# Performance work log

Measured on AMD Instinct MI355X. Metric: run time of the kernel, lower is better.

The kernel has to match this reference:

```python
import jax, jax.numpy as jnp
import numpy as np

N_NODES = 100000
N_EDGES = 1250000
D = 64
K = 5
EPS = 1e-8


def setup_inputs() -> dict:
    key = jax.random.key(0)
    k1, k2, k3, k4 = jax.random.split(key, 4)
    x = jax.random.normal(k1, (N_NODES, D), dtype=jnp.float32)
    mask = jax.random.normal(k2, (N_NODES, 1), dtype=jnp.float32)
    edge_index = jax.random.randint(k3, (2, N_EDGES), 0, N_NODES, dtype=jnp.int64)
    # orthogonal-ish init for the linear layer (QR of gaussian), gain for tanh = 5/3
    g = jax.random.normal(k4, (D, D), dtype=jnp.float32)
    q, _ = jnp.linalg.qr(g)
    W = (5.0 / 3.0) * q.astype(jnp.float32)
    b = jnp.zeros((D,), dtype=jnp.float32)
    alpha = jnp.float32(0.001)
    return {"x": x, "mask": mask, "edge_index": edge_index, "W": W, "b": b, "alpha": alpha}


def _forward(x, mask, edge_index, W, b, alpha):
    n = x.shape[0]
    # x_fn: Linear + Tanh
    h = jnp.tanh(x @ W.T + b)  # [N, D]
    src = edge_index[0]
    dst = edge_index[1]
    hs = h[src]  # [E, D] gather
    hd = h[dst]  # [E, D] gather
    # torch cosine_similarity with eps clamp on each norm
    ns = jnp.maximum(jnp.sqrt(jnp.sum(hs * hs, axis=-1)), EPS)
    nd = jnp.maximum(jnp.sqrt(jnp.sum(hd * hd, axis=-1)), EPS)
    cos = jnp.sum(hs * hd, axis=-1) / (ns * nd)
    edge_weights = jax.nn.relu(cos)  # [E]

    # gcn_norm with self loops (PyG APPNP default): D^-1/2 (A + I) D^-1/2
    loop = jnp.arange(n, dtype=src.dtype)
    row = jnp.concatenate([src, loop])
    col = jnp.concatenate([dst, loop])
    w = jnp.concatenate([edge_weights, jnp.ones((n,), dtype=edge_weights.dtype)])
    deg = jax.ops.segment_sum(w, col, num_segments=n)
    dis = jnp.where(deg > 0, jax.lax.rsqrt(jnp.maximum(deg, EPS)), 0.0)
    norm_w = dis[row] * w * dis[col]  # [E + N]

    # APPNP: K steps of f = (1-alpha) * A_hat @ f + alpha * f0
    f0 = jax.nn.relu(mask)  # [N, 1]
    f = f0
    for _ in range(K):
        msg = norm_w[:, None] * f[row]  # gather + weight
        agg = jax.ops.segment_sum(msg, col, num_segments=n)  # scatter-add
        f = (1.0 - alpha) * agg + alpha * f0
    return f, edge_weights


def reference(x, mask, edge_index, W, b, alpha):
    return _forward(x, mask, edge_index, W, b, alpha)
```

## Files before the change

### kernel.cpp

```cpp
#include <hip/hip_runtime.h>
#include <hip/hip_fp16.h>
#include <math.h>

#define N_NODES 100000
#define N_EDGES 1250000
#define D 64
#define EPS 1e-8f

#define ZERO_BLOCKS 391
#define GEMM_BLOCKS 1024
#define NODE_BLOCKS 391
#define COSR_BLOCKS 9766

__global__ __launch_bounds__(256) void k_gemm_zero(
    const float* __restrict__ x, const float* __restrict__ W,
    const float* __restrict__ b, __half* __restrict__ hn,
    unsigned long long* __restrict__ cnt64)
{
    if (blockIdx.x < ZERO_BLOCKS) {
        int i = blockIdx.x * 256 + threadIdx.x;
        if (i < N_NODES) cnt64[i] = 0ULL;
        return;
    }
    __shared__ float xrow[4][72];
    const int lane = threadIdx.x & 63;
    const int wid  = threadIdx.x >> 6;

    float Wreg[64];
    const float4* Wv = (const float4*)(W + lane * D);
    #pragma unroll
    for (int q = 0; q < 16; ++q) {
        float4 w4 = Wv[q];
        Wreg[4*q+0] = w4.x; Wreg[4*q+1] = w4.y;
        Wreg[4*q+2] = w4.z; Wreg[4*q+3] = w4.w;
    }
    const float bj = b[lane];
    float* xl = xrow[wid];

    const int wave   = (blockIdx.x - ZERO_BLOCKS) * 4 + wid;
    const int nwaves = GEMM_BLOCKS * 4;

    for (int row = wave; row < N_NODES; row += nwaves) {
        float xv = x[(size_t)row * D + lane];
        xl[lane] = xv;
        float acc = bj;
        #pragma unroll
        for (int q = 0; q < 16; ++q) {
            float4 xk4 = *(const float4*)(xl + 4*q);
            acc = fmaf(xk4.x, Wreg[4*q+0], acc);
            acc = fmaf(xk4.y, Wreg[4*q+1], acc);
            acc = fmaf(xk4.z, Wreg[4*q+2], acc);
            acc = fmaf(xk4.w, Wreg[4*q+3], acc);
        }
        float h = tanhf(acc);
        float s = h * h;
        #pragma unroll
        for (int m = 32; m >= 1; m >>= 1) s += __shfl_xor(s, m, 64);
        float nrm = fmaxf(sqrtf(s), EPS);
        hn[(size_t)row * D + lane] = __float2half_rn(h / nrm);
    }
}

__device__ __forceinline__ float dot8h(float4 a, float4 c)
{
    const __half2* ah = (const __half2*)&a;
    const __half2* ch = (const __half2*)&c;
    float p = 0.0f;
    #pragma unroll
    for (int q = 0; q < 4; ++q) {
        float2 af = __half22float2(ah[q]);
        float2 cf = __half22float2(ch[q]);
        p = fmaf(af.x, cf.x, p);
        p = fmaf(af.y, cf.y, p);
    }
    return p;
}

__global__ __launch_bounds__(256) void k_cos_rank(
    const int* __restrict__ ei, const __half* __restrict__ hn,
    unsigned long long* __restrict__ cnt64, int* __restrict__ rank,
    float* __restrict__ wout)
{
    int t = blockIdx.x * 256 + threadIdx.x;
    int g = t >> 3, sub = t & 7;
    if (g >= N_EDGES / 4) return;
    int e0 = g * 4;
    int4 ss = *(const int4*)(ei + e0);
    int4 dd = *(const int4*)(ei + N_EDGES + e0);

    float4 a0 = ((const float4*)(hn + (size_t)ss.x * D))[sub];
    float4 c0 = ((const float4*)(hn + (size_t)dd.x * D))[sub];
    float4 a1 = ((const float4*)(hn + (size_t)ss.y * D))[sub];
    float4 c1 = ((const float4*)(hn + (size_t)dd.y * D))[sub];
    float4 a2 = ((const float4*)(hn + (size_t)ss.z * D))[sub];
    float4 c2 = ((const float4*)(hn + (size_t)dd.z * D))[sub];
    float4 a3 = ((const float4*)(hn + (size_t)ss.w * D))[sub];
    float4 c3 = ((const float4*)(hn + (size_t)dd.w * D))[sub];

    float p0 = dot8h(a0, c0);
    float p1 = dot8h(a1, c1);
    float p2 = dot8h(a2, c2);
    float p3 = dot8h(a3, c3);
    p0 += __shfl_xor(p0, 1, 64);  p1 += __shfl_xor(p1, 1, 64);
    p2 += __shfl_xor(p2, 1, 64);  p3 += __shfl_xor(p3, 1, 64);
    p0 += __shfl_xor(p0, 2, 64);  p1 += __shfl_xor(p1, 2, 64);
    p2 += __shfl_xor(p2, 2, 64);  p3 += __shfl_xor(p3, 2, 64);
    p0 += __shfl_xor(p0, 4, 64);  p1 += __shfl_xor(p1, 4, 64);
    p2 += __shfl_xor(p2, 4, 64);  p3 += __shfl_xor(p3, 4, 64);

    float w0 = fmaxf(p0, 0.0f);
    float w1 = fmaxf(p1, 0.0f);
    float w2 = fmaxf(p2, 0.0f);
    float w3 = fmaxf(p3, 0.0f);

    if (sub == 0) {
        *(float4*)(wout + e0) = make_float4(w0, w1, w2, w3);
    }
    if (sub < 4) {
        float w = (sub == 0) ? w0 : (sub == 1) ? w1 : (sub == 2) ? w2 : w3;
        int   d = (sub == 0) ? dd.x : (sub == 1) ? dd.y : (sub == 2) ? dd.z : dd.w;
        if (w > 0.0f) {
            unsigned long long pack =
                (1ULL << 40) | (unsigned long long)(w * 4294967296.0f);
            unsigned long long old = atomicAdd(cnt64 + d, pack);
            rank[e0 + sub] = (int)(old >> 40);
        }
    }
}

__device__ __forceinline__ int wave_iscan(int v, int lane)
{
    int incl = v;
    #pragma unroll
    for (int m = 1; m < 64; m <<= 1) {
        int o = __shfl_up(incl, m, 64);
        if (lane >= m) incl += o;
    }
    return incl;
}

__global__ __launch_bounds__(256) void k_scan1(
    const unsigned long long* __restrict__ cnt64, int* __restrict__ rowptr,
    int* __restrict__ bsum, const float* __restrict__ mask,
    float* __restrict__ dis, float* __restrict__ y)
{
    __shared__ int wsum[4];
    int t = threadIdx.x, b = blockIdx.x;
    int i = b * 256 + t;
    int lane = t & 63, wid = t >> 6;
    unsigned long long pv = (i < N_NODES) ? cnt64[i] : 0ULL;
    int v = (int)(pv >> 40);
    if (i < N_NODES) {
        float degsum = (float)(pv & 0xFFFFFFFFFFULL) * 2.3283064365386963e-10f;
        float di = rsqrtf(fmaxf(degsum + 1.0f, EPS));
        dis[i] = di;
        y[i] = di * fmaxf(mask[i], 0.0f);
    }
    int incl = wave_iscan(v, lane);
    if (lane == 63) wsum[wid] = incl;
    __syncthreads();
    int off = 0;
    #pragma unroll
    for (int k = 0; k < 4; ++k) if (k < wid) off += wsum[k];
    if (i < N_NODES) rowptr[i] = off + incl - v;
    if (t == 255) bsum[b] = off + incl;
}

__global__ __launch_bounds__(512) void k_scan2(
    const int* __restrict__ bsum, int* __restrict__ boff, int nblk,
    int* __restrict__ rowptr)
{
    __shared__ int wsum[8];
    int t = threadIdx.x;
    int lane = t & 63, wid = t >> 6;
    int v = (t < nblk) ? bsum[t] : 0;
    int incl = wave_iscan(v, lane);
    if (lane == 63) wsum[wid] = incl;
    __syncthreads();
    int off = 0;
    #pragma unroll
    for (int k = 0; k < 8; ++k) if (k < wid) off += wsum[k];
    if (t < nblk) boff[t] = off + incl - v;
    if (t == nblk - 1) rowptr[N_NODES] = off + incl;
}

__global__ __launch_bounds__(256) void k_place(
    const int* __restrict__ ei, const int* __restrict__ rank_pos,
    const int* __restrict__ rowptr, const int* __restrict__ boff,
    const float* __restrict__ wsrc, int2* __restrict__ pairs)
{
    int e = blockIdx.x * 256 + threadIdx.x;
    if (e >= N_EDGES) return;
    float w = wsrc[e];
    if (!(w > 0.0f)) return;
    int s = ei[e];
    int d = ei[N_EDGES + e];
    int pos = rowptr[d] + boff[d >> 8] + rank_pos[e];
    pairs[pos] = make_int2(s, __float_as_int(w));
}

__global__ __launch_bounds__(256) void k_spmv(
    const int* __restrict__ rowptr, const int* __restrict__ boff,
    const int2* __restrict__ pairs,
    const float* __restrict__ y_in, const float* __restrict__ dis,
    const float* __restrict__ mask, const float* __restrict__ alpha_p,
    float* __restrict__ y_out, float* __restrict__ f_out)
{
    int t = blockIdx.x * 256 + threadIdx.x;
    int node = t >> 2, l = t & 3;
    if (node >= N_NODES) return;
    int beg = rowptr[node] + boff[node >> 8];
    int np1 = node + 1;
    int end = rowptr[np1] + (np1 < N_NODES ? boff[np1 >> 8] : 0);
    float sum = 0.0f;
    for (int j = beg + l; j < end; j += 8) {
        int2 p0 = pairs[j];
        int j2 = j + 4;
        int2 p1 = make_int2(0, 0);
        if (j2 < end) p1 = pairs[j2];
        sum += __int_as_float(p0.y) * y_in[p0.x];
        sum += __int_as_float(p1.y) * y_in[p1.x];
    }
    sum += __shfl_xor(sum, 1, 64);
    sum += __shfl_xor(sum, 2, 64);
    if (l == 0) {
        float di = dis[node];
        float alpha = alpha_p[0];
        float f0 = fmaxf(mask[node], 0.0f);
        float fn = (1.0f - alpha) * di * (sum + y_in[node]) + alpha * f0;
        if (f_out) f_out[node] = fn;
        y_out[node] = di * fn;
    }
}

extern "C" void kernel_launch(void* const* d_in, const int* in_sizes, int n_in,
                              void* d_out, int out_size, void* d_ws, size_t ws_size,
                              hipStream_t stream)
{
    const float* x     = (const float*)d_in[0];
    const float* mask  = (const float*)d_in[1];
    const int*   ei    = (const int*)  d_in[2];
    const float* W     = (const float*)d_in[3];
    const float* b     = (const float*)d_in[4];
    const float* alpha = (const float*)d_in[5];

    float* out_f = (float*)d_out;
    float* out_w = (float*)d_out + N_NODES;

    float* ws = (float*)d_ws;
    __half* hn    = (__half*)ws;
    int2*  pairs  = (int2*) (ws + 3200000);
    int*   rank   = (int*)  (ws + 5700000);
    unsigned long long* cnt64 = (unsigned long long*)(ws + 6950000);
    int*   rowptr = (int*)  (ws + 7150000);
    float* dis    =          ws + 7250016;
    float* y_a    =          ws + 7350016;
    float* y_b    =          ws + 7450016;
    int*   bsum   = (int*)  (ws + 7550016);
    int*   boff   = (int*)  (ws + 7550528);

    const int edgeBlocks = (N_EDGES + 255) / 256;
    const int segBlocks  = (int)(((long long)N_NODES * 4 + 255) / 256);

    k_gemm_zero<<<ZERO_BLOCKS + GEMM_BLOCKS, 256, 0, stream>>>(x, W, b, hn, cnt64);
    k_cos_rank<<<COSR_BLOCKS, 256, 0, stream>>>(ei, hn, cnt64, rank, out_w);
    k_scan1<<<NODE_BLOCKS, 256, 0, stream>>>(cnt64, rowptr, bsum, mask, dis, y_a);
    k_scan2<<<1, 512, 0, stream>>>(bsum, boff, NODE_BLOCKS, rowptr);
    k_place<<<edgeBlocks, 256, 0, stream>>>(ei, rank, rowptr, boff, out_w, pairs);

    k_spmv<<<segBlocks, 256, 0, stream>>>(rowptr, boff, pairs, y_a, dis, mask, alpha, y_b, (float*)nullptr);
    k_spmv<<<segBlocks, 256, 0, stream>>>(rowptr, boff, pairs, y_b, dis, mask, alpha, y_a, (float*)nullptr);
    k_spmv<<<segBlocks, 256, 0, stream>>>(rowptr, boff, pairs, y_a, dis, mask, alpha, y_b, (float*)nullptr);
    k_spmv<<<segBlocks, 256, 0, stream>>>(rowptr, boff, pairs, y_b, dis, mask, alpha, y_a, (float*)nullptr);
    k_spmv<<<segBlocks, 256, 0, stream>>>(rowptr, boff, pairs, y_a, dis, mask, alpha, y_b, out_f);
}
```

Before: 202.8 us.

## Pack CSR pairs into 32-bit words with 15-bit quantized weights

```diff
diff --git a/kernel.cpp b/kernel.cpp
--- a/kernel.cpp
+++ b/kernel.cpp
@@ -78,7 +78,7 @@
 
 __global__ __launch_bounds__(256) void k_cos_rank(
     const int* __restrict__ ei, const __half* __restrict__ hn,
-    unsigned long long* __restrict__ cnt64, int* __restrict__ rank,
+    unsigned long long* __restrict__ cnt64, unsigned char* __restrict__ rank,
     float* __restrict__ wout)
 {
     int t = blockIdx.x * 256 + threadIdx.x;
@@ -123,7 +123,7 @@
             unsigned long long pack =
                 (1ULL << 40) | (unsigned long long)(w * 4294967296.0f);
             unsigned long long old = atomicAdd(cnt64 + d, pack);
-            rank[e0 + sub] = (int)(old >> 40);
+            rank[e0 + sub] = (unsigned char)(old >> 40);
         }
     }
 }
@@ -142,7 +142,8 @@
 __global__ __launch_bounds__(256) void k_scan1(
     const unsigned long long* __restrict__ cnt64, int* __restrict__ rowptr,
     int* __restrict__ bsum, const float* __restrict__ mask,
-    float* __restrict__ dis, float* __restrict__ y)
+    const float* __restrict__ alpha_p, float* __restrict__ dis,
+    float* __restrict__ y, float* __restrict__ Ac, float* __restrict__ Bc)
 {
     __shared__ int wsum[4];
     int t = threadIdx.x, b = blockIdx.x;
@@ -153,8 +154,12 @@
     if (i < N_NODES) {
         float degsum = (float)(pv & 0xFFFFFFFFFFULL) * 2.3283064365386963e-10f;
         float di = rsqrtf(fmaxf(degsum + 1.0f, EPS));
+        float al = alpha_p[0];
+        float m0 = fmaxf(mask[i], 0.0f);
         dis[i] = di;
-        y[i] = di * fmaxf(mask[i], 0.0f);
+        y[i]   = di * m0;
+        Ac[i]  = (1.0f - al) * di * di;
+        Bc[i]  = al * di * m0;
     }
     int incl = wave_iscan(v, lane);
     if (lane == 63) wsum[wid] = incl;
@@ -185,9 +190,9 @@
 }
 
 __global__ __launch_bounds__(256) void k_place(
-    const int* __restrict__ ei, const int* __restrict__ rank_pos,
+    const int* __restrict__ ei, const unsigned char* __restrict__ rank_pos,
     const int* __restrict__ rowptr, const int* __restrict__ boff,
-    const float* __restrict__ wsrc, int2* __restrict__ pairs)
+    const float* __restrict__ wsrc, unsigned int* __restrict__ pairs)
 {
     int e = blockIdx.x * 256 + threadIdx.x;
     if (e >= N_EDGES) return;
@@ -195,16 +200,17 @@
     if (!(w > 0.0f)) return;
     int s = ei[e];
     int d = ei[N_EDGES + e];
-    int pos = rowptr[d] + boff[d >> 8] + rank_pos[e];
-    pairs[pos] = make_int2(s, __float_as_int(w));
-}
-
-__global__ __launch_bounds__(256) void k_spmv(
+    int pos = rowptr[d] + boff[d >> 8] + (int)rank_pos[e];
+    unsigned int wq = (unsigned int)(w * 32767.0f + 0.5f);
+    if (wq > 32767u) wq = 32767u;
+    pairs[pos] = ((unsigned int)s << 15) | wq;
+}
+
+__global__ __launch_bounds__(256) void k_spmv_fast(
     const int* __restrict__ rowptr, const int* __restrict__ boff,
-    const int2* __restrict__ pairs,
-    const float* __restrict__ y_in, const float* __restrict__ dis,
-    const float* __restrict__ mask, const float* __restrict__ alpha_p,
-    float* __restrict__ y_out, float* __restrict__ f_out)
+    const unsigned int* __restrict__ pairs,
+    const float* __restrict__ y_in, const float* __restrict__ Ac,
+    const float* __restrict__ Bc, float* __restrict__ y_out)
 {
     int t = blockIdx.x * 256 + threadIdx.x;
     int node = t >> 2, l = t & 3;
@@ -214,12 +220,41 @@
     int end = rowptr[np1] + (np1 < N_NODES ? boff[np1 >> 8] : 0);
     float sum = 0.0f;
     for (int j = beg + l; j < end; j += 8) {
-        int2 p0 = pairs[j];
+        unsigned int p0 = pairs[j];
         int j2 = j + 4;
-        int2 p1 = make_int2(0, 0);
+        unsigned int p1 = 0;
         if (j2 < end) p1 = pairs[j2];
-        sum += __int_as_float(p0.y) * y_in[p0.x];
-        sum += __int_as_float(p1.y) * y_in[p1.x];
+        sum = fmaf((float)(p0 & 0x7FFFu), y_in[p0 >> 15], sum * 32767.0f) * (1.0f/32767.0f);
+        sum = fmaf((float)(p1 & 0x7FFFu), y_in[p1 >> 15], sum * 32767.0f) * (1.0f/32767.0f);
+    }
+    sum += __shfl_xor(sum, 1, 64);
+    sum += __shfl_xor(sum, 2, 64);
+    if (l == 0) {
+        y_out[node] = fmaf(Ac[node], sum + y_in[node], Bc[node]);
+    }
+}
+
+__global__ __launch_bounds__(256) void k_spmv_last(
+    const int* __restrict__ rowptr, const int* __restrict__ boff,
+    const unsigned int* __restrict__ pairs,
+    const float* __restrict__ y_in, const float* __restrict__ dis,
+    const float* __restrict__ mask, const float* __restrict__ alpha_p,
+    float* __restrict__ f_out)
+{
+    int t = blockIdx.x * 256 + threadIdx.x;
+    int node = t >> 2, l = t & 3;
+    if (node >= N_NODES) return;
+    int beg = rowptr[node] + boff[node >> 8];
+    int np1 = node + 1;
+    int end = rowptr[np1] + (np1 < N_NODES ? boff[np1 >> 8] : 0);
+    float sum = 0.0f;
+    for (int j = beg + l; j < end; j += 8) {
+        unsigned int p0 = pairs[j];
+        int j2 = j + 4;
+        unsigned int p1 = 0;
+        if (j2 < end) p1 = pairs[j2];
+        sum = fmaf((float)(p0 & 0x7FFFu), y_in[p0 >> 15], sum * 32767.0f) * (1.0f/32767.0f);
+        sum = fmaf((float)(p1 & 0x7FFFu), y_in[p1 >> 15], sum * 32767.0f) * (1.0f/32767.0f);
     }
     sum += __shfl_xor(sum, 1, 64);
     sum += __shfl_xor(sum, 2, 64);
@@ -227,9 +262,7 @@
         float di = dis[node];
         float alpha = alpha_p[0];
         float f0 = fmaxf(mask[node], 0.0f);
-        float fn = (1.0f - alpha) * di * (sum + y_in[node]) + alpha * f0;
-        if (f_out) f_out[node] = fn;
-        y_out[node] = di * fn;
+        f_out[node] = (1.0f - alpha) * di * (sum + y_in[node]) + alpha * f0;
     }
 }
 
@@ -249,28 +282,31 @@
 
     float* ws = (float*)d_ws;
     __half* hn    = (__half*)ws;
-    int2*  pairs  = (int2*) (ws + 3200000);
-    int*   rank   = (int*)  (ws + 5700000);
-    unsigned long long* cnt64 = (unsigned long long*)(ws + 6950000);
-    int*   rowptr = (int*)  (ws + 7150000);
-    float* dis    =          ws + 7250016;
-    float* y_a    =          ws + 7350016;
-    float* y_b    =          ws + 7450016;
-    int*   bsum   = (int*)  (ws + 7550016);
-    int*   boff   = (int*)  (ws + 7550528);
+    unsigned int* pairs = (unsigned int*)(ws + 3200000);
+    unsigned char* rank = (unsigned char*)(ws + 4450000);
+    unsigned long long* cnt64 = (unsigned long long*)(ws + 4770000);
+    int*   rowptr = (int*)  (ws + 4970000);
+    float* dis    =          ws + 5070016;
+    float* y_a    =          ws + 5170016;
+    float* y_b    =          ws + 5270016;
+    float* Acoef  =          ws + 5370016;
+    float* Bcoef  =          ws + 5470016;
+    int*   bsum   = (int*)  (ws + 5570016);
+    int*   boff   = (int*)  (ws + 5570528);
 
     const int edgeBlocks = (N_EDGES + 255) / 256;
     const int segBlocks  = (int)(((long long)N_NODES * 4 + 255) / 256);
 
     k_gemm_zero<<<ZERO_BLOCKS + GEMM_BLOCKS, 256, 0, stream>>>(x, W, b, hn, cnt64);
     k_cos_rank<<<COSR_BLOCKS, 256, 0, stream>>>(ei, hn, cnt64, rank, out_w);
-    k_scan1<<<NODE_BLOCKS, 256, 0, stream>>>(cnt64, rowptr, bsum, mask, dis, y_a);
+    k_scan1<<<NODE_BLOCKS, 256, 0, stream>>>(cnt64, rowptr, bsum, mask, alpha,
+                                             dis, y_a, Acoef, Bcoef);
     k_scan2<<<1, 512, 0, stream>>>(bsum, boff, NODE_BLOCKS, rowptr);
     k_place<<<edgeBlocks, 256, 0, stream>>>(ei, rank, rowptr, boff, out_w, pairs);
 
-    k_spmv<<<segBlocks, 256, 0, stream>>>(rowptr, boff, pairs, y_a, dis, mask, alpha, y_b, (float*)nullptr);
-    k_spmv<<<segBlocks, 256, 0, stream>>>(rowptr, boff, pairs, y_b, dis, mask, alpha, y_a, (float*)nullptr);
-    k_spmv<<<segBlocks, 256, 0, stream>>>(rowptr, boff, pairs, y_a, dis, mask, alpha, y_b, (float*)nullptr);
-    k_spmv<<<segBlocks, 256, 0, stream>>>(rowptr, boff, pairs, y_b, dis, mask, alpha, y_a, (float*)nullptr);
-    k_spmv<<<segBlocks, 256, 0, stream>>>(rowptr, boff, pairs, y_a, dis, mask, alpha, y_b, out_f);
-}
+    k_spmv_fast<<<segBlocks, 256, 0, stream>>>(rowptr, boff, pairs, y_a, Acoef, Bcoef, y_b);
+    k_spmv_fast<<<segBlocks, 256, 0, stream>>>(rowptr, boff, pairs, y_b, Acoef, Bcoef, y_a);
+    k_spmv_fast<<<segBlocks, 256, 0, stream>>>(rowptr, boff, pairs, y_a, Acoef, Bcoef, y_b);
+    k_spmv_fast<<<segBlocks, 256, 0, stream>>>(rowptr, boff, pairs, y_b, Acoef, Bcoef, y_a);
+    k_spmv_last<<<segBlocks, 256, 0, stream>>>(rowptr, boff, pairs, y_a, dis, mask, alpha, out_f);
+}
```

Result: no change. 202.2 us (-0.3%).
